# Kernel tuning notes

Hardware: AMD Instinct MI355X
Metric: run time of the kernel (lower is better)

The kernel has to match this reference:

```python
import jax, jax.numpy as jnp
import numpy as np
from jax import lax

P = 8  # patch size

def _to_patches(x):
    # [B,C,H,W] -> [B,C,H//P,W//P,P,P]
    b, c, h, w = x.shape
    x = x.reshape(b, c, h // P, P, w // P, P)
    return x.transpose(0, 1, 2, 4, 3, 5)

def _from_patches(x):
    # [B,C,h,w,P,P] -> [B,C,h*P,w*P]
    b, c, h, w, p1, p2 = x.shape
    return x.transpose(0, 1, 2, 4, 3, 5).reshape(b, c, h * p1, w * p2)

def setup_inputs() -> dict:
    key = jax.random.key(0)
    ks = jax.random.split(key, 7)
    B, C = 4, 64
    H = W = 256
    HID2 = 2 * C  # hidden_features * 2 with expansion factor 1
    img = jax.random.normal(ks[0], (B, C, H, W), dtype=jnp.float32)
    event = jax.random.normal(ks[1], (B, C, H, W), dtype=jnp.float32)
    # conv weights (no bias), OIHW
    w_img = jax.random.normal(ks[2], (HID2, C, 1, 1), dtype=jnp.float32) * (1.0 / np.sqrt(C))
    w_event = jax.random.normal(ks[3], (HID2, C, 1, 1), dtype=jnp.float32) * (1.0 / np.sqrt(C))
    w_dw = jax.random.normal(ks[4], (HID2, 1, 3, 3), dtype=jnp.float32) * (1.0 / 3.0)
    fft_filter = jnp.ones((HID2, 1, 1, P, P // 2 + 1), dtype=jnp.float32)  # init = ones, as in module
    w_out = jax.random.normal(ks[5], (C, C, 1, 1), dtype=jnp.float32) * (1.0 / np.sqrt(C))
    return {"img": img, "event": event, "w_img": w_img, "w_event": w_event,
            "w_dw": w_dw, "fft_filter": fft_filter, "w_out": w_out}

def reference(img, event, w_img, w_event, w_dw, fft_filter, w_out):
    hid2 = w_img.shape[0]
    # 1x1 input convs (no bias) as einsum
    img_ = jnp.einsum('bchw,oc->bohw', img, w_img[:, :, 0, 0])
    event_ = jnp.einsum('bchw,oc->bohw', event, w_event[:, :, 0, 0])
    # 8x8 patchwise rfft2
    img_fft = jnp.fft.rfft2(_to_patches(img_))        # [B,2C,h,w,8,5] complex
    event_fft = jnp.fft.rfft2(_to_patches(event_))
    event_fft = event_fft * fft_filter                 # filter broadcasts over h,w
    x_fft = img_fft * event_fft + event_fft
    x_patch = jnp.fft.irfft2(x_fft, s=(P, P))
    x = _from_patches(x_patch)                          # [B,2C,H,W]
    # depthwise 3x3 conv, groups = 2C
    x = lax.conv_general_dilated(x, w_dw, window_strides=(1, 1), padding='SAME',
                                 feature_group_count=hid2,
                                 dimension_numbers=('NCHW', 'OIHW', 'NCHW'))
    x1, x2 = jnp.split(x, 2, axis=1)
    x = jax.nn.gelu(x1, approximate=False) * x2
    # 1x1 project out
    return jnp.einsum('bchw,oc->bohw', x, w_out[:, :, 0, 0])
```

## Files before the change

### kernel.cpp

```cpp
#include <hip/hip_runtime.h>
#include <math.h>

typedef unsigned short u16;
typedef unsigned int   u32;

#define S2 0.70710678118654752440f

typedef float f32x4 __attribute__((ext_vector_type(4)));
typedef short bf16x8 __attribute__((ext_vector_type(8)));
typedef float f32x2 __attribute__((ext_vector_type(2)));
typedef __bf16 bf16x2 __attribute__((ext_vector_type(2)));
#define MFMA(a,b,c) __builtin_amdgcn_mfma_f32_16x16x32_bf16(a,b,c,0,0,0)

__device__ __forceinline__ float bf2f(u16 u){
  union { u32 i; float f; } v; v.i = ((u32)u) << 16; return v.f;
}
__device__ __forceinline__ u16 f2bf(float f){
  union { __bf16 b; u16 u; } v; v.b = (__bf16)f; return v.u;
}
__device__ __forceinline__ u32 pk_bf16(float lo, float hi){
  f32x2 s; s.x = lo; s.y = hi;
  union { bf16x2 h; u32 u; } v;
  v.h = __builtin_convertvector(s, bf16x2);
  return v.u;
}

struct C2 { float r, i; };

__device__ __forceinline__ void fft8_fwd(C2* y){
  C2 a0 = {y[0].r+y[4].r, y[0].i+y[4].i};
  C2 a1 = {y[0].r-y[4].r, y[0].i-y[4].i};
  C2 a2 = {y[2].r+y[6].r, y[2].i+y[6].i};
  C2 a3 = {y[2].r-y[6].r, y[2].i-y[6].i};
  C2 b0 = {y[1].r+y[5].r, y[1].i+y[5].i};
  C2 b1 = {y[1].r-y[5].r, y[1].i-y[5].i};
  C2 b2 = {y[3].r+y[7].r, y[3].i+y[7].i};
  C2 b3 = {y[3].r-y[7].r, y[3].i-y[7].i};
  C2 E0 = {a0.r+a2.r, a0.i+a2.i};
  C2 E2 = {a0.r-a2.r, a0.i-a2.i};
  C2 E1 = {a1.r+a3.i, a1.i-a3.r};
  C2 E3 = {a1.r-a3.i, a1.i+a3.r};
  C2 O0 = {b0.r+b2.r, b0.i+b2.i};
  C2 O2 = {b0.r-b2.r, b0.i-b2.i};
  C2 O1 = {b1.r+b3.i, b1.i-b3.r};
  C2 O3 = {b1.r-b3.i, b1.i+b3.r};
  C2 t1 = {S2*(O1.r+O1.i), S2*(O1.i-O1.r)};
  C2 t2 = {O2.i, -O2.r};
  C2 t3 = {S2*(O3.i-O3.r), -S2*(O3.r+O3.i)};
  y[0].r=E0.r+O0.r; y[0].i=E0.i+O0.i;
  y[4].r=E0.r-O0.r; y[4].i=E0.i-O0.i;
  y[1].r=E1.r+t1.r; y[1].i=E1.i+t1.i;
  y[5].r=E1.r-t1.r; y[5].i=E1.i-t1.i;
  y[2].r=E2.r+t2.r; y[2].i=E2.i+t2.i;
  y[6].r=E2.r-t2.r; y[6].i=E2.i-t2.i;
  y[3].r=E3.r+t3.r; y[3].i=E3.i+t3.i;
  y[7].r=E3.r-t3.r; y[7].i=E3.i-t3.i;
}

__device__ __forceinline__ void fft8_inv(C2* z){
  C2 A0 = {z[0].r+z[4].r, z[0].i+z[4].i};
  C2 A1 = {z[1].r+z[5].r, z[1].i+z[5].i};
  C2 A2 = {z[2].r+z[6].r, z[2].i+z[6].i};
  C2 A3 = {z[3].r+z[7].r, z[3].i+z[7].i};
  C2 D0 = {z[0].r-z[4].r, z[0].i-z[4].i};
  C2 D1 = {z[1].r-z[5].r, z[1].i-z[5].i};
  C2 D2 = {z[2].r-z[6].r, z[2].i-z[6].i};
  C2 D3 = {z[3].r-z[7].r, z[3].i-z[7].i};
  C2 B0 = D0;
  C2 B1 = {S2*(D1.r-D1.i), S2*(D1.i+D1.r)};
  C2 B2 = {-D2.i, D2.r};
  C2 B3 = {-S2*(D3.r+D3.i), S2*(D3.r-D3.i)};
  z[0].r = A0.r+A1.r+A2.r+A3.r;           z[0].i = A0.i+A1.i+A2.i+A3.i;
  z[2].r = A0.r-A2.r-(A1.i-A3.i);         z[2].i = A0.i-A2.i+(A1.r-A3.r);
  z[4].r = A0.r-A1.r+A2.r-A3.r;           z[4].i = A0.i-A1.i+A2.i-A3.i;
  z[6].r = A0.r-A2.r+(A1.i-A3.i);         z[6].i = A0.i-A2.i-(A1.r-A3.r);
  z[1].r = B0.r+B1.r+B2.r+B3.r;           z[1].i = B0.i+B1.i+B2.i+B3.i;
  z[3].r = B0.r-B2.r-(B1.i-B3.i);         z[3].i = B0.i-B2.i+(B1.r-B3.r);
  z[5].r = B0.r-B1.r+B2.r-B3.r;           z[5].i = B0.i-B1.i+B2.i-B3.i;
  z[7].r = B0.r-B2.r+(B1.i-B3.i);         z[7].i = B0.i-B2.i-(B1.r-B3.r);
}

__device__ __forceinline__ void rfft8_row(float* x){
  float et0=x[0]+x[4], et1=x[0]-x[4], et2=x[2]+x[6], et3=x[2]-x[6];
  float ot0=x[1]+x[5], ot1=x[1]-x[5], ot2=x[3]+x[7], ot3=x[3]-x[7];
  float E0=et0+et2, E2=et0-et2;
  float O0=ot0+ot2, O2=ot0-ot2;
  float om=S2*(ot1-ot3), op=S2*(ot1+ot3);
  x[0]=E0+O0;  x[1]=E0-O0;
  x[2]=et1+om; x[3]=-et3-op;
  x[4]=E2;     x[5]=-O2;
  x[6]=et1-om; x[7]=et3-op;
}

__device__ __forceinline__ void irfft8_row(float f0, C2 R1, C2 R2, C2 R3, float f4, float* x){
  float A0  = f0+f4, B0v = f0-f4;
  float A1r = R1.r+R3.r, A1i = R1.i-R3.i;
  float A2  = 2.f*R2.r;
  float D1r = R1.r-R3.r, D1i = R1.i+R3.i;
  float B1r = S2*(D1r-D1i), B1i = S2*(D1i+D1r);
  float B2  = -2.f*R2.i;
  const float k = 1.f/64.f;
  x[0]=k*(A0 +A2+2.f*A1r); x[2]=k*(A0 -A2-2.f*A1i);
  x[4]=k*(A0 +A2-2.f*A1r); x[6]=k*(A0 -A2+2.f*A1i);
  x[1]=k*(B0v+B2+2.f*B1r); x[3]=k*(B0v-B2-2.f*B1i);
  x[5]=k*(B0v+B2-2.f*B1r); x[7]=k*(B0v-B2+2.f*B1i);
}

__global__ void k_prep(const float* __restrict__ wi, const float* __restrict__ we,
                       const float* __restrict__ wo,
                       u16* __restrict__ wbi, u16* __restrict__ wbe, u16* __restrict__ wbo){
  int i = blockIdx.x*256 + threadIdx.x;
  if (i < 8192)        wbi[i]        = f2bf(wi[i]);
  else if (i < 16384)  wbe[i-8192]   = f2bf(we[i-8192]);
  else if (i < 20480)  wbo[i-16384]  = f2bf(wo[i-16384]);
}

__global__ __launch_bounds__(256, 2)
void k_front(const float* __restrict__ img, const float* __restrict__ evt,
             const u16* __restrict__ wbi, const u16* __restrict__ wbe,
             const float* __restrict__ filt, u16* __restrict__ yout){
  __shared__ __align__(16) u16 s_a[8192];
  __shared__ __align__(16) u16 s_spec[16384];

  const int t   = threadIdx.x;
  const int bid = blockIdx.x;
  const int b   = bid >> 9;
  const int ph  = (bid >> 4) & 31;
  const int bx  = bid & 15;
  const int wv   = t >> 6;
  const int quad = (t >> 4) & 3;
  const int ln15 = t & 15;
  const int pc   = t >> 7;
  const int c    = t & 127;

  auto do_stage = [&](const float* src){
    #pragma unroll
    for (int i=0;i<8;i++){
      int task = t + 256*i;
      int ci = task>>5, q = task&31;
      int r = q>>2, j = q&3;
      const float4 v = *(const float4*)(src +
          (((size_t)(b*64+ci)*256 + ph*8 + r)*256 + bx*16 + j*4));
      int p0 = (j>>1)*64 + r*8 + (j&1)*4;
      int gbase = ci>>3, cl = ci&7;
      float vv[4] = {v.x, v.y, v.z, v.w};
      #pragma unroll
      for (int w=0;w<4;w++){
        int p = p0+w;
        int g = gbase ^ (p&7) ^ r;
        s_a[p*64 + g*8 + cl] = f2bf(vv[w]);
      }
    }
  };

  auto do_gemm = [&](const u16* __restrict__ wb){
    f32x4 acc[2][8];
    #pragma unroll
    for (int nt=0;nt<2;nt++)
      #pragma unroll
      for (int mt=0;mt<8;mt++)
        acc[nt][mt] = (f32x4){0.f,0.f,0.f,0.f};
    const int nb = wv*32;
    #pragma unroll
    for (int kk=0;kk<2;kk++){
      bf16x8 bf0 = *(const bf16x8*)&wb[(nb      + ln15)*64 + kk*32 + quad*8];
      bf16x8 bf1 = *(const bf16x8*)&wb[(nb + 16 + ln15)*64 + kk*32 + quad*8];
      #pragma unroll
      for (int mt=0;mt<8;mt++){
        int pix = mt*16 + ln15;
        int g = (kk*4+quad) ^ (pix&7) ^ ((pix>>3)&7);
        bf16x8 af = *(const bf16x8*)&s_a[pix*64 + g*8];
        acc[0][mt] = MFMA(af, bf0, acc[0][mt]);
        acc[1][mt] = MFMA(af, bf1, acc[1][mt]);
      }
    }
    #pragma unroll
    for (int nt=0;nt<2;nt++){
      int och = nb + nt*16 + ln15;
      #pragma unroll
      for (int mt=0;mt<8;mt++){
        int p0 = mt*16 + quad*4;
        f32x4 v = acc[nt][mt];
        u32 lo = pk_bf16(v.x, v.y);
        u32 hi = pk_bf16(v.z, v.w);
        int d = (p0>>3) ^ (och&7);
        u32* dst = (u32*)&s_spec[och*128 + d*8 + (p0&7)];
        dst[0] = lo; dst[1] = hi;
      }
    }
  };

  auto read_spec = [&](float* p){
    #pragma unroll
    for (int d=0; d<8; d++){
      int cz = (pc*8+d) ^ (c&7);
      const uint4 q4 = *(const uint4*)&s_spec[c*128 + cz*8];
      u32 ws4[4] = {q4.x, q4.y, q4.z, q4.w};
      #pragma unroll
      for (int e=0;e<4;e++){
        p[d*8+2*e]   = bf2f((u16)(ws4[e] & 0xFFFFu));
        p[d*8+2*e+1] = bf2f((u16)(ws4[e] >> 16));
      }
    }
  };

  do_stage(evt);
  __syncthreads();
  do_gemm(wbe);
  __syncthreads();

  float pe[64];
  read_spec(pe);
  #pragma unroll
  for (int r=0;r<8;r++) rfft8_row(&pe[r*8]);

  do_stage(img);
  __syncthreads();
  do_gemm(wbi);
  __syncthreads();

  float pi[64];
  read_spec(pi);
  __syncthreads();
  #pragma unroll
  for (int r=0;r<8;r++) rfft8_row(&pi[r*8]);

  C2 X[8][5];
  {
    const float* fl = filt + c*40;
    #pragma unroll
    for (int j=0;j<5;j++){
      C2 e8[8], i8[8];
      #pragma unroll
      for (int r=0;r<8;r++){
        float re_e, im_e, re_i, im_i;
        if (j==0){ re_e=pe[r*8];   im_e=0.f; re_i=pi[r*8];   im_i=0.f; }
        else if (j==4){ re_e=pe[r*8+1]; im_e=0.f; re_i=pi[r*8+1]; im_i=0.f; }
        else { re_e=pe[r*8+2*j]; im_e=pe[r*8+2*j+1];
               re_i=pi[r*8+2*j]; im_i=pi[r*8+2*j+1]; }
        e8[r].r=re_e; e8[r].i=im_e; i8[r].r=re_i; i8[r].i=im_i;
      }
      fft8_fwd(e8);
      fft8_fwd(i8);
      #pragma unroll
      for (int ky=0;ky<8;ky++){
        float f  = fl[ky*5+j];
        float fr = e8[ky].r*f, fi2 = e8[ky].i*f;
        X[ky][j].r = i8[ky].r*fr - i8[ky].i*fi2 + fr;
        X[ky][j].i = i8[ky].r*fi2 + i8[ky].i*fr + fi2;
      }
    }
    #pragma unroll
    for (int j=0;j<5;j++){
      C2 z[8];
      #pragma unroll
      for (int ky=0;ky<8;ky++) z[ky] = X[ky][j];
      fft8_inv(z);
      #pragma unroll
      for (int ky=0;ky<8;ky++) X[ky][j] = z[ky];
    }
  }

  {
    const int cp = (c&31) | ((c&32)<<1) | ((c&64)>>1);
    #pragma unroll
    for (int r=0;r<8;r++){
      float xr[8];
      irfft8_row(X[r][0].r, X[r][1], X[r][2], X[r][3], X[r][4].r, xr);
      #pragma unroll
      for (int n2=0;n2<8;n2++)
        s_spec[(pc*64 + r*8 + n2)*128 + cp] = f2bf(xr[n2]);
    }
  }
  __syncthreads();

  {
    const uint4* sg = (const uint4*)s_spec;
    uint4* dst = (uint4*)(yout + (size_t)(b*1024 + ph*32 + bx*2)*8192);
    #pragma unroll
    for (int i=0;i<8;i++){
      int q2 = t + 256*i;
      dst[q2] = sg[q2];
    }
  }
}

__global__ __launch_bounds__(256, 2)
void k_back(const u16* __restrict__ y, const float* __restrict__ wdw,
            const u16* __restrict__ wbo, float* __restrict__ out){
  __shared__ __align__(16) u16 L[18*19*68];
  __shared__ __align__(16) u16 A[256*32];

  const int t   = threadIdx.x;
  const int bid = blockIdx.x;
  const int b   = bid >> 8;
  const int ty  = (bid >> 4) & 15;
  const int tx  = bid & 15;
  const int wv   = t >> 6;
  const int quad = (t >> 4) & 3;
  const int ln15 = t & 15;
  const int y_  = t >> 4, x_ = t & 15;
  const int sw  = (t&3) ^ ((t>>2)&3);

  f32x4 acc[4][4];
  #pragma unroll
  for (int mt=0;mt<4;mt++)
    #pragma unroll
    for (int nt=0;nt<4;nt++)
      acc[mt][nt] = (f32x4){0.f,0.f,0.f,0.f};

  for (int chunk=0; chunk<2; chunk++){
    for (int i=0;i<11;i++){
      int task = t + 256*i;
      if (task < 2592){
        int q = task & 7, pix = task >> 3;
        int py = pix/18, px = pix - py*18;
        int gy = ty*16 - 1 + py, gx = tx*16 - 1 + px;
        uint4 v = make_uint4(0u,0u,0u,0u);
        if ((unsigned)gy < 256u && (unsigned)gx < 256u){
          int phh = gy>>3, pww = gx>>3, k = (gy&7)*8 + (gx&7);
          v = *(const uint4*)&y[(((size_t)(b*1024 + phh*32 + pww))*64 + k)*128
                                + chunk*64 + q*8];
        }
        int ad = (py*19+px)*68 + q*8;
        *(uint2*)&L[ad]     = make_uint2(v.x, v.y);
        *(uint2*)&L[ad + 4] = make_uint2(v.z, v.w);
      }
    }
    __syncthreads();

    #pragma unroll
    for (int cg=0; cg<8; cg++){
      float d1[4] = {0.f,0.f,0.f,0.f};
      float d2[4] = {0.f,0.f,0.f,0.f};
      const float* w1p = wdw + (chunk*32 + cg*4)*9;
      const float* w2p = wdw + (64 + chunk*32 + cg*4)*9;
      #pragma unroll
      for (int dy=0; dy<3; dy++)
        #pragma unroll
        for (int dx=0; dx<3; dx++){
          int base = ((y_+dy)*19 + (x_+dx))*68;
          const uint2 a1 = *(const uint2*)&L[base + cg*4];
          const uint2 a2 = *(const uint2*)&L[base + 32 + cg*4];
          const float* wp1 = w1p + dy*3 + dx;
          const float* wp2 = w2p + dy*3 + dx;
          d1[0] = fmaf(wp1[0],  bf2f((u16)(a1.x & 0xFFFFu)), d1[0]);
          d1[1] = fmaf(wp1[9],  bf2f((u16)(a1.x >> 16)),     d1[1]);
          d1[2] = fmaf(wp1[18], bf2f((u16)(a1.y & 0xFFFFu)), d1[2]);
          d1[3] = fmaf(wp1[27], bf2f((u16)(a1.y >> 16)),     d1[3]);
          d2[0] = fmaf(wp2[0],  bf2f((u16)(a2.x & 0xFFFFu)), d2[0]);
          d2[1] = fmaf(wp2[9],  bf2f((u16)(a2.x >> 16)),     d2[1]);
          d2[2] = fmaf(wp2[18], bf2f((u16)(a2.y & 0xFFFFu)), d2[2]);
          d2[3] = fmaf(wp2[27], bf2f((u16)(a2.y >> 16)),     d2[3]);
        }
      float gg[4];
      #pragma unroll
      for (int l=0;l<4;l++){
        float g1 = d1[l];
        float g = 0.5f * g1 * (1.f + erff(g1 * 0.70710678118654752f));
        gg[l] = g * d2[l];
      }
      int pos = ((cg>>1) ^ sw)*8 + (cg&1)*4;
      *(uint2*)&A[t*32 + pos] =
          make_uint2(pk_bf16(gg[0], gg[1]), pk_bf16(gg[2], gg[3]));
    }
    __syncthreads();

    bf16x8 bfr[4];
    #pragma unroll
    for (int nt=0;nt<4;nt++)
      bfr[nt] = *(const bf16x8*)&wbo[(nt*16 + ln15)*64 + chunk*32 + quad*8];
    #pragma unroll
    for (int mt=0;mt<4;mt++){
      int px8 = wv*64 + mt*16 + ln15;
      int q2 = quad ^ ((px8&3) ^ ((px8>>2)&3));
      bf16x8 af = *(const bf16x8*)&A[px8*32 + q2*8];
      #pragma unroll
      for (int nt=0;nt<4;nt++)
        acc[mt][nt] = MFMA(af, bfr[nt], acc[mt][nt]);
    }
    __syncthreads();
  }

  #pragma unroll
  for (int mt=0;mt<4;mt++){
    int row = ty*16 + wv*4 + mt;
    #pragma unroll
    for (int nt=0;nt<4;nt++){
      int och = nt*16 + ln15;
      f32x4 v = acc[mt][nt];
      float4 o4 = make_float4(v.x, v.y, v.z, v.w);
      *(float4*)(out + (((size_t)(b*64 + och))*256 + row)*256 + tx*16 + quad*4) = o4;
    }
  }
}

extern "C" void kernel_launch(void* const* d_in, const int* in_sizes, int n_in,
                              void* d_out, int out_size, void* d_ws, size_t ws_size,
                              hipStream_t stream){
  const float* img   = (const float*)d_in[0];
  const float* evt   = (const float*)d_in[1];
  const float* w_img = (const float*)d_in[2];
  const float* w_evt = (const float*)d_in[3];
  const float* w_dw  = (const float*)d_in[4];
  const float* filt  = (const float*)d_in[5];
  const float* w_out = (const float*)d_in[6];
  float* out = (float*)d_out;

  u16* wbi = (u16*)d_ws;
  u16* wbe = (u16*)((char*)d_ws + 16384);
  u16* wbo = (u16*)((char*)d_ws + 32768);
  u16* y   = (u16*)((char*)d_ws + 65536);

  k_prep<<<80, 256, 0, stream>>>(w_img, w_evt, w_out, wbi, wbe, wbo);
  k_front<<<2048, 256, 0, stream>>>(img, evt, wbi, wbe, filt, y);
  k_back<<<1024, 256, 0, stream>>>(y, w_dw, wbo, out);
}
```

Before: 300.3 us.

## Prefetch staged inputs into registers to overlap loads with compute; use tanh GELU

In the front kernel, the image tile's global loads are issued before the event spectrum FFT work and written to shared memory afterwards. This hides load latency. In the back kernel, the halo load for the second channel chunk is split into a register load and a shared-memory write, so the load overlaps the first chunk's depthwise conv and GEMM. Exact erf GELU is replaced by the tanh approximation built on fast exp and rcp, which changes the numerics slightly. The extra registers held in flight raise pressure and may limit occupancy or cause spills.

```diff
diff --git a/kernel.cpp b/kernel.cpp
--- a/kernel.cpp
+++ b/kernel.cpp
@@ -133,17 +133,25 @@
   const int pc   = t >> 7;
   const int c    = t & 127;
 
-  auto do_stage = [&](const float* src){
+  auto stage_load = [&](const float* src, float4* v){
     #pragma unroll
     for (int i=0;i<8;i++){
       int task = t + 256*i;
       int ci = task>>5, q = task&31;
       int r = q>>2, j = q&3;
-      const float4 v = *(const float4*)(src +
+      v[i] = *(const float4*)(src +
           (((size_t)(b*64+ci)*256 + ph*8 + r)*256 + bx*16 + j*4));
+    }
+  };
+  auto stage_write = [&](const float4* v){
+    #pragma unroll
+    for (int i=0;i<8;i++){
+      int task = t + 256*i;
+      int ci = task>>5, q = task&31;
+      int r = q>>2, j = q&3;
       int p0 = (j>>1)*64 + r*8 + (j&1)*4;
       int gbase = ci>>3, cl = ci&7;
-      float vv[4] = {v.x, v.y, v.z, v.w};
+      float vv[4] = {v[i].x, v[i].y, v[i].z, v[i].w};
       #pragma unroll
       for (int w=0;w<4;w++){
         int p = p0+w;
@@ -204,17 +212,24 @@
     }
   };
 
-  do_stage(evt);
+  {
+    float4 sv[8];
+    stage_load(evt, sv);
+    stage_write(sv);
+  }
   __syncthreads();
   do_gemm(wbe);
   __syncthreads();
+
+  float4 sv[8];
+  stage_load(img, sv);
 
   float pe[64];
   read_spec(pe);
   #pragma unroll
   for (int r=0;r<8;r++) rfft8_row(&pe[r*8]);
 
-  do_stage(img);
+  stage_write(sv);
   __syncthreads();
   do_gemm(wbi);
   __syncthreads();
@@ -302,33 +317,39 @@
   const int y_  = t >> 4, x_ = t & 15;
   const int sw  = (t&3) ^ ((t>>2)&3);
 
-  f32x4 acc[4][4];
-  #pragma unroll
-  for (int mt=0;mt<4;mt++)
-    #pragma unroll
-    for (int nt=0;nt<4;nt++)
-      acc[mt][nt] = (f32x4){0.f,0.f,0.f,0.f};
-
-  for (int chunk=0; chunk<2; chunk++){
+  auto halo_load = [&](int chunk, uint4* hv){
+    #pragma unroll
+    for (int i=0;i<11;i++){
+      int task = t + 256*i;
+      uint4 v = make_uint4(0u,0u,0u,0u);
+      if (task < 2592){
+        int q = task & 7, pix = task >> 3;
+        int py = pix/18, px = pix - py*18;
+        int gy = ty*16 - 1 + py, gx = tx*16 - 1 + px;
+        if ((unsigned)gy < 256u && (unsigned)gx < 256u){
+          int phh = gy>>3, pww = gx>>3, k = (gy&7)*8 + (gx&7);
+          v = *(const uint4*)&y[(((size_t)(b*1024 + phh*32 + pww))*64 + k)*128
+                                + chunk*64 + q*8];
+        }
+      }
+      hv[i] = v;
+    }
+  };
+  auto halo_write = [&](const uint4* hv){
+    #pragma unroll
     for (int i=0;i<11;i++){
       int task = t + 256*i;
       if (task < 2592){
         int q = task & 7, pix = task >> 3;
         int py = pix/18, px = pix - py*18;
-        int gy = ty*16 - 1 + py, gx = tx*16 - 1 + px;
-        uint4 v = make_uint4(0u,0u,0u,0u);
-        if ((unsigned)gy < 256u && (unsigned)gx < 256u){
-          int phh = gy>>3, pww = gx>>3, k = (gy&7)*8 + (gx&7);
-          v = *(const uint4*)&y[(((size_t)(b*1024 + phh*32 + pww))*64 + k)*128
-                                + chunk*64 + q*8];
-        }
         int ad = (py*19+px)*68 + q*8;
-        *(uint2*)&L[ad]     = make_uint2(v.x, v.y);
-        *(uint2*)&L[ad + 4] = make_uint2(v.z, v.w);
-      }
-    }
-    __syncthreads();
-
+        *(uint2*)&L[ad]     = make_uint2(hv[i].x, hv[i].y);
+        *(uint2*)&L[ad + 4] = make_uint2(hv[i].z, hv[i].w);
+      }
+    }
+  };
+
+  auto dwconv = [&](int chunk){
     #pragma unroll
     for (int cg=0; cg<8; cg++){
       float d1[4] = {0.f,0.f,0.f,0.f};
@@ -357,15 +378,19 @@
       #pragma unroll
       for (int l=0;l<4;l++){
         float g1 = d1[l];
-        float g = 0.5f * g1 * (1.f + erff(g1 * 0.70710678118654752f));
+        float u  = 0.7978845608028654f * fmaf(0.044715f*g1*g1, g1, g1);
+        float e  = __expf(2.f*u);
+        float th = 1.f - 2.f*__builtin_amdgcn_rcpf(e + 1.f);
+        float g  = 0.5f * g1 * (1.f + th);
         gg[l] = g * d2[l];
       }
       int pos = ((cg>>1) ^ sw)*8 + (cg&1)*4;
       *(uint2*)&A[t*32 + pos] =
           make_uint2(pk_bf16(gg[0], gg[1]), pk_bf16(gg[2], gg[3]));
     }
-    __syncthreads();
-
+  };
+
+  auto do_gemm = [&](int chunk, f32x4 (&acc)[4][4]){
     bf16x8 bfr[4];
     #pragma unroll
     for (int nt=0;nt<4;nt++)
@@ -379,8 +404,30 @@
       for (int nt=0;nt<4;nt++)
         acc[mt][nt] = MFMA(af, bfr[nt], acc[mt][nt]);
     }
-    __syncthreads();
-  }
+  };
+
+  f32x4 acc[4][4];
+  #pragma unroll
+  for (int mt=0;mt<4;mt++)
+    #pragma unroll
+    for (int nt=0;nt<4;nt++)
+      acc[mt][nt] = (f32x4){0.f,0.f,0.f,0.f};
+
+  uint4 hv[11];
+  halo_load(0, hv);
+  halo_write(hv);
+  __syncthreads();
+
+  halo_load(1, hv);
+  dwconv(0);
+  __syncthreads();
+  do_gemm(0, acc);
+  halo_write(hv);
+  __syncthreads();
+
+  dwconv(1);
+  __syncthreads();
+  do_gemm(1, acc);
 
   #pragma unroll
   for (int mt=0;mt<4;mt++){
```

Result: faster. 292.9 us (-2.5%).
